# Performance work log

Hardware: AMD Instinct MI355X
Metric: run time of the kernel (lower is better)

Reference implementation:

```python
import jax, jax.numpy as jnp
import numpy as np

ALPHA = 0.5
PATH_LEN = 7  # 1 start entity + 3 (module, entity) hops
NUM_ENTITIES = 200000
EMBED = 128
NUM_MOD = 64
HIDDEN = 512
OUT_DIM = 64
BATCH = 8192


def setup_inputs() -> dict:
    key = jax.random.key(0)
    ks = jax.random.split(key, 8)
    stdv = 1.0 / np.sqrt(EMBED)
    return {
        "entity_embeds": jax.random.normal(ks[0], (NUM_ENTITIES, EMBED), jnp.float32) * 0.05,
        "W_mods": jax.random.uniform(ks[1], (NUM_MOD, EMBED, EMBED), jnp.float32, -stdv, stdv),
        "W1": jax.random.normal(ks[2], (HIDDEN, EMBED), jnp.float32) * stdv,
        "b1": jax.random.normal(ks[3], (HIDDEN,), jnp.float32) * 0.01,
        "W2": jax.random.normal(ks[4], (OUT_DIM, HIDDEN), jnp.float32) * (1.0 / np.sqrt(HIDDEN)),
        "b2": jax.random.normal(ks[5], (OUT_DIM,), jnp.float32) * 0.01,
        "entity_ids": jax.random.randint(ks[6], (BATCH, 4), 0, NUM_ENTITIES, jnp.int64 if jax.config.jax_enable_x64 else jnp.int32),
        "module_ids": jax.random.randint(ks[7], (BATCH, 3), 0, NUM_MOD, jnp.int64 if jax.config.jax_enable_x64 else jnp.int32),
    }


def reference(entity_embeds, W_mods, W1, b1, W2, b2, entity_ids, module_ids):
    # Batched version of ModuleNet.forward over a batch of fixed-length-7 paths.
    x = entity_embeds[entity_ids[:, 0]]  # [B, E] start entity embedding
    bias = x
    for h in range(3):  # hops over (module_id, entity_id) pairs
        Wm = W_mods[module_ids[:, h]]          # [B, E, E] per-row weight gather
        bias = entity_embeds[entity_ids[:, h + 1]]  # [B, E]
        x = jax.nn.relu(jnp.einsum('boi,bi->bo', Wm, x) + bias)
    w = 1.0 / (PATH_LEN * ALPHA)
    out = (1.0 - w) * bias + w * x  # [B, E]
    # classifier: Linear -> ReLU -> Linear
    h1 = jax.nn.relu(out @ W1.T + b1)
    logits = h1 @ W2.T + b2  # [B, OUT_DIM]
    return logits
```

## Files before the change

### kernel.cpp

```cpp
#include <hip/hip_runtime.h>

namespace {

typedef short bf16x8 __attribute__((ext_vector_type(8)));
typedef float f32x4 __attribute__((ext_vector_type(4)));

constexpr int BATCH = 8192;
constexpr int NMOD  = 64;
constexpr int CAP   = 256;
constexpr int CSTR  = 16;
constexpr float WB  = 1.0f / (7.0f * 0.5f);

constexpr size_t OFF_WHI = 0;
constexpr size_t OFF_WLO = 524288;
constexpr size_t OFF_XH0 = 1048576;
constexpr size_t OFF_XL0 = 1572864;
constexpr size_t OFF_XH1 = 2097152;
constexpr size_t OFF_XL1 = 2621440;
constexpr size_t OFF_W1H = 3145728;
constexpr size_t OFF_W1L = 3178496;
constexpr size_t OFF_W2H = 3211264;
constexpr size_t OFF_W2L = 3227648;
constexpr size_t OFF_CNT = 3244032;
constexpr size_t OFF_BKT = 3247104;

__device__ __forceinline__ ushort f2bf(float x) {
  unsigned u = __builtin_bit_cast(unsigned, x);
  u += 0x7FFFu + ((u >> 16) & 1u);
  return (ushort)(u >> 16);
}
__device__ __forceinline__ float bf2f(ushort h) {
  return __builtin_bit_cast(float, ((unsigned)h) << 16);
}
__device__ __forceinline__ void cvt8(const float* v, bf16x8& hi, bf16x8& lo) {
#pragma unroll
  for (int j = 0; j < 8; ++j) {
    const float x = v[j];
    const ushort h = f2bf(x);
    hi[j] = (short)h;
    lo[j] = (short)f2bf(x - bf2f(h));
  }
}

__global__ __launch_bounds__(256) void k_prep(const float* __restrict__ Wm,
                                              const float* __restrict__ W1,
                                              const float* __restrict__ W2,
                                              const int* __restrict__ mids,
                                              float* __restrict__ ws) {
  const int bx = blockIdx.x;
  const int tid = threadIdx.x;
  if (bx < 560) {
    const float* src;
    ushort *dh, *dl;
    size_t i8;
    if (bx < 512) {
      src = Wm; dh = (ushort*)(ws + OFF_WHI); dl = (ushort*)(ws + OFF_WLO);
      i8 = (size_t)bx * 256 + tid;
    } else if (bx < 544) {
      src = W1; dh = (ushort*)(ws + OFF_W1H); dl = (ushort*)(ws + OFF_W1L);
      i8 = (size_t)(bx - 512) * 256 + tid;
    } else {
      src = W2; dh = (ushort*)(ws + OFF_W2H); dl = (ushort*)(ws + OFF_W2L);
      i8 = (size_t)(bx - 544) * 256 + tid;
    }
    float v[8];
    *(float4*)&v[0] = *(const float4*)&src[i8 * 8];
    *(float4*)&v[4] = *(const float4*)&src[i8 * 8 + 4];
    bf16x8 hi, lo;
    cvt8(v, hi, lo);
    *(bf16x8*)&dh[i8 * 8] = hi;
    *(bf16x8*)&dl[i8 * 8] = lo;
  } else {
    const int idx = (bx - 560) * 256 + tid;
    if (idx < BATCH * 3) {
      const int b = idx / 3, h = idx - b * 3;
      const int m = mids[idx];
      int* cnt = (int*)(ws + OFF_CNT);
      int* bkt = (int*)(ws + OFF_BKT);
      const int pos = atomicAdd(&cnt[(h * NMOD + m) * CSTR], 1);
      bkt[(h * NMOD + m) * CAP + pos] = b;
    }
  }
}

template <int HOP>
__global__ __launch_bounds__(256, 2) void k_hop(const float* __restrict__ E,
                                                const int* __restrict__ eids,
                                                float* __restrict__ ws) {
  const int m = blockIdx.x >> 2, sl = blockIdx.x & 3;
  const int cn = ((const int*)(ws + OFF_CNT))[(HOP * NMOD + m) * CSTR];
  const int r0 = sl * 64;
  if (r0 >= cn) return;
  const int nr = min(64, cn - r0);

  __shared__ ushort wh[128 * 72];
  __shared__ ushort wl[128 * 72];
  __shared__ int rows[64], esrc[64], ebia[64];

  const int tid = threadIdx.x;
  const ushort* WhiG = (const ushort*)(ws + OFF_WHI) + (size_t)m * 16384;
  const ushort* WloG = (const ushort*)(ws + OFF_WLO) + (size_t)m * 16384;
  const int* bkt = (const int*)(ws + OFF_BKT) + (HOP * NMOD + m) * CAP + r0;
  const ushort* XHp = (const ushort*)(ws + (HOP == 2 ? OFF_XH1 : OFF_XH0));
  const ushort* XLp = (const ushort*)(ws + (HOP == 2 ? OFF_XL1 : OFF_XL0));
  ushort* XHn = (ushort*)(ws + (HOP == 1 ? OFF_XH1 : OFF_XH0));
  ushort* XLn = (ushort*)(ws + (HOP == 1 ? OFF_XL1 : OFF_XL0));

  if (tid < 64) {
    const int b = bkt[tid < nr ? tid : 0];
    rows[tid] = b;
    esrc[tid] = (HOP == 0) ? eids[b * 4] : b;
    ebia[tid] = eids[b * 4 + HOP + 1];
  }

  const int w = tid >> 6, l = tid & 63;
  const int lg = l >> 4, lr = l & 15;
  const int g0 = (w & 1) * 2, f0 = (w >> 1) * 4;

  f32x4 acc[2][4] = {};

#pragma unroll
  for (int p = 0; p < 2; ++p) {
    __syncthreads();
    for (int e = tid; e < 128 * 8; e += 256) {
      const int c = e >> 3, s = e & 7;
      *(bf16x8*)&wh[c * 72 + s * 8] =
          *(const bf16x8*)&WhiG[(size_t)c * 128 + p * 64 + s * 8];
      *(bf16x8*)&wl[c * 72 + s * 8] =
          *(const bf16x8*)&WloG[(size_t)c * 128 + p * 64 + s * 8];
    }
    __syncthreads();

    bf16x8 ah[2][2], al[2][2];
#pragma unroll
    for (int g = 0; g < 2; ++g) {
      const int row = (g0 + g) * 16 + lr;
#pragma unroll
      for (int s = 0; s < 2; ++s) {
        const int k0 = p * 64 + s * 32 + lg * 8;
        if (HOP == 0) {
          const float* sp = E + (size_t)esrc[row] * 128;
          float v[8];
          *(float4*)&v[0] = *(const float4*)&sp[k0];
          *(float4*)&v[4] = *(const float4*)&sp[k0 + 4];
          cvt8(v, ah[g][s], al[g][s]);
        } else {
          const size_t xo = (size_t)esrc[row] * 128 + k0;
          ah[g][s] = *(const bf16x8*)&XHp[xo];
          al[g][s] = *(const bf16x8*)&XLp[xo];
        }
      }
    }

#pragma unroll
    for (int f = 0; f < 4; ++f) {
      const int c = (f0 + f) * 16 + lr;
#pragma unroll
      for (int s = 0; s < 2; ++s) {
        const bf16x8 bh = *(const bf16x8*)&wh[c * 72 + s * 32 + lg * 8];
        const bf16x8 bl = *(const bf16x8*)&wl[c * 72 + s * 32 + lg * 8];
#pragma unroll
        for (int g = 0; g < 2; ++g) {
          acc[g][f] = __builtin_amdgcn_mfma_f32_16x16x32_bf16(ah[g][s], bh, acc[g][f], 0, 0, 0);
          acc[g][f] = __builtin_amdgcn_mfma_f32_16x16x32_bf16(al[g][s], bh, acc[g][f], 0, 0, 0);
          acc[g][f] = __builtin_amdgcn_mfma_f32_16x16x32_bf16(ah[g][s], bl, acc[g][f], 0, 0, 0);
        }
      }
    }
  }

#pragma unroll
  for (int g = 0; g < 2; ++g) {
#pragma unroll
    for (int q = 0; q < 4; ++q) {
      const int row = (g0 + g) * 16 + lg * 4 + q;
      if (row < nr) {
        const int b = rows[row];
        const float* bp = E + (size_t)ebia[row] * 128;
        const size_t ob = (size_t)b * 128;
#pragma unroll
        for (int f = 0; f < 4; ++f) {
          const int col = (f0 + f) * 16 + lr;
          const float bias = bp[col];
          float v = fmaxf(acc[g][f][q] + bias, 0.f);
          if (HOP == 2) v = (1.f - WB) * bias + WB * v;
          const ushort h = f2bf(v);
          XHn[ob + col] = h;
          XLn[ob + col] = f2bf(v - bf2f(h));
        }
      }
    }
  }
}

constexpr int HSTR = 520;
constexpr int WSTR = 136;
__global__ __launch_bounds__(256, 2) void k_mlp(const float* __restrict__ b1,
                                                const float* __restrict__ b2,
                                                float* __restrict__ ws,
                                                float* __restrict__ out) {
  __shared__ ushort w1h[64 * WSTR];
  __shared__ ushort w1l[64 * WSTR];
  __shared__ ushort hh[16 * HSTR];
  __shared__ ushort hl[16 * HSTR];
  const int tid = threadIdx.x;
  const int row0 = blockIdx.x * 16;
  const ushort* XH = (const ushort*)(ws + OFF_XH0);
  const ushort* XL = (const ushort*)(ws + OFF_XL0);
  const ushort* W1H = (const ushort*)(ws + OFF_W1H);
  const ushort* W1L = (const ushort*)(ws + OFF_W1L);
  const ushort* W2H = (const ushort*)(ws + OFF_W2H);
  const ushort* W2L = (const ushort*)(ws + OFF_W2L);

  const int w = tid >> 6, l = tid & 63;
  const int lg = l >> 4, lr = l & 15;

  bf16x8 ah[4], al[4];
#pragma unroll
  for (int s = 0; s < 4; ++s) {
    const size_t xo = (size_t)(row0 + lr) * 128 + s * 32 + lg * 8;
    ah[s] = *(const bf16x8*)&XH[xo];
    al[s] = *(const bf16x8*)&XL[xo];
  }

  for (int ch = 0; ch < 8; ++ch) {
    __syncthreads();
    for (int e = tid; e < 64 * 16; e += 256) {
      const int c = e >> 4, s8 = e & 15;
      const size_t go = (size_t)(ch * 64 + c) * 128 + s8 * 8;
      *(bf16x8*)&w1h[c * WSTR + s8 * 8] = *(const bf16x8*)&W1H[go];
      *(bf16x8*)&w1l[c * WSTR + s8 * 8] = *(const bf16x8*)&W1L[go];
    }
    __syncthreads();

    const int cl = w * 16 + lr;
    f32x4 a = {};
#pragma unroll
    for (int s = 0; s < 4; ++s) {
      const bf16x8 bh = *(const bf16x8*)&w1h[cl * WSTR + s * 32 + lg * 8];
      const bf16x8 bl = *(const bf16x8*)&w1l[cl * WSTR + s * 32 + lg * 8];
      a = __builtin_amdgcn_mfma_f32_16x16x32_bf16(ah[s], bh, a, 0, 0, 0);
      a = __builtin_amdgcn_mfma_f32_16x16x32_bf16(al[s], bh, a, 0, 0, 0);
      a = __builtin_amdgcn_mfma_f32_16x16x32_bf16(ah[s], bl, a, 0, 0, 0);
    }
    const int c = ch * 64 + w * 16 + lr;
    const float bb = b1[c];
#pragma unroll
    for (int q = 0; q < 4; ++q) {
      const int r = lg * 4 + q;
      const float v = fmaxf(a[q] + bb, 0.f);
      const ushort h = f2bf(v);
      hh[r * HSTR + c] = h;
      hl[r * HSTR + c] = f2bf(v - bf2f(h));
    }
  }
  __syncthreads();

  f32x4 acc2 = {};
#pragma unroll 4
  for (int s = 0; s < 16; ++s) {
    const size_t wo = (size_t)(w * 16 + lr) * 512 + s * 32 + lg * 8;
    const bf16x8 a2h = *(const bf16x8*)&W2H[wo];
    const bf16x8 a2l = *(const bf16x8*)&W2L[wo];
    const int ko = s * 32 + lg * 8;
    const bf16x8 b2h = *(const bf16x8*)&hh[lr * HSTR + ko];
    const bf16x8 b2l = *(const bf16x8*)&hl[lr * HSTR + ko];
    acc2 = __builtin_amdgcn_mfma_f32_16x16x32_bf16(a2h, b2h, acc2, 0, 0, 0);
    acc2 = __builtin_amdgcn_mfma_f32_16x16x32_bf16(a2l, b2h, acc2, 0, 0, 0);
    acc2 = __builtin_amdgcn_mfma_f32_16x16x32_bf16(a2h, b2l, acc2, 0, 0, 0);
  }
  const float4 bb2 = *(const float4*)&b2[w * 16 + lg * 4];
  float4 o;
  o.x = acc2[0] + bb2.x;
  o.y = acc2[1] + bb2.y;
  o.z = acc2[2] + bb2.z;
  o.w = acc2[3] + bb2.w;
  *(float4*)&out[(size_t)(row0 + lr) * 64 + w * 16 + lg * 4] = o;
}

}

extern "C" void kernel_launch(void* const* d_in, const int* in_sizes, int n_in,
                              void* d_out, int out_size, void* d_ws,
                              size_t ws_size, hipStream_t stream) {
  const float* E  = (const float*)d_in[0];
  const float* Wm = (const float*)d_in[1];
  const float* W1 = (const float*)d_in[2];
  const float* b1 = (const float*)d_in[3];
  const float* W2 = (const float*)d_in[4];
  const float* b2 = (const float*)d_in[5];
  const int* eids = (const int*)d_in[6];
  const int* mids = (const int*)d_in[7];
  float* out = (float*)d_out;
  float* ws = (float*)d_ws;

  (void)hipMemsetAsync((char*)d_ws + OFF_CNT * sizeof(float), 0,
                       192 * CSTR * sizeof(int), stream);
  k_prep<<<dim3(656), dim3(256), 0, stream>>>(Wm, W1, W2, mids, ws);
  k_hop<0><<<dim3(256), dim3(256), 0, stream>>>(E, eids, ws);
  k_hop<1><<<dim3(256), dim3(256), 0, stream>>>(E, eids, ws);
  k_hop<2><<<dim3(256), dim3(256), 0, stream>>>(E, eids, ws);
  k_mlp<<<dim3(512), dim3(256), 0, stream>>>(b1, b2, ws, out);
}
```

Baseline: 79.80 us.

## Fuse hop 0 and bucketing into prep kernel, replacing atomics with ballot compaction

Hop 0 now runs inside the prep kernel. Its blocks rebuild their own bucket rows by scanning module ids with ballot prefix sums and convert the module weights to hi/lo bf16 on the fly, so they no longer depend on the prepared workspace. Bucketing for hops 1 and 2 uses per-(hop, module) blocks with deterministic ballot compaction instead of atomics, which removes the memset. Together this drops one launch and one memset, but each block scans all 8192 ids, which adds redundant reads and serial loop work per block.

```diff
diff --git a/kernel.cpp b/kernel.cpp
--- a/kernel.cpp
+++ b/kernel.cpp
@@ -42,13 +42,18 @@
   }
 }
 
-__global__ __launch_bounds__(256) void k_prep(const float* __restrict__ Wm,
-                                              const float* __restrict__ W1,
-                                              const float* __restrict__ W2,
-                                              const int* __restrict__ mids,
-                                              float* __restrict__ ws) {
+__global__ __launch_bounds__(256, 2) void k_prep(
+    const float* __restrict__ E, const float* __restrict__ Wm,
+    const float* __restrict__ W1, const float* __restrict__ W2,
+    const int* __restrict__ eids, const int* __restrict__ mids,
+    float* __restrict__ ws) {
+  __shared__ ushort wh[128 * 72];
+  __shared__ ushort wl[128 * 72];
+  __shared__ int rows[64], esrc[64], ebia[64];
+  __shared__ int wsum[4];
   const int bx = blockIdx.x;
   const int tid = threadIdx.x;
+
   if (bx < 560) {
     const float* src;
     ushort *dh, *dl;
@@ -70,15 +75,145 @@
     cvt8(v, hi, lo);
     *(bf16x8*)&dh[i8 * 8] = hi;
     *(bf16x8*)&dl[i8 * 8] = lo;
-  } else {
-    const int idx = (bx - 560) * 256 + tid;
-    if (idx < BATCH * 3) {
-      const int b = idx / 3, h = idx - b * 3;
-      const int m = mids[idx];
-      int* cnt = (int*)(ws + OFF_CNT);
-      int* bkt = (int*)(ws + OFF_BKT);
-      const int pos = atomicAdd(&cnt[(h * NMOD + m) * CSTR], 1);
-      bkt[(h * NMOD + m) * CAP + pos] = b;
+    return;
+  }
+
+  if (bx < 688) {
+    const int hm64 = bx - 560;
+    const int h = 1 + (hm64 >> 6), m = hm64 & 63;
+    const int hm = h * NMOD + m;
+    int* cnt = (int*)(ws + OFF_CNT);
+    int* bkt = (int*)(ws + OFF_BKT) + hm * CAP;
+    const int wv = tid >> 6, ln = tid & 63;
+    int count = 0;
+    for (int it = 0; it < BATCH / 256; ++it) {
+      const int b = it * 256 + tid;
+      const bool hit = (mids[b * 3 + h] == m);
+      const unsigned long long mask = __ballot(hit);
+      const int pre = __popcll(mask & ((1ull << ln) - 1ull));
+      if (ln == 0) wsum[wv] = __popcll(mask);
+      __syncthreads();
+      int wbase = count;
+#pragma unroll
+      for (int u = 0; u < 4; ++u)
+        if (u < wv) wbase += wsum[u];
+      if (hit) bkt[wbase + pre] = b;
+      count += wsum[0] + wsum[1] + wsum[2] + wsum[3];
+      __syncthreads();
+    }
+    if (tid == 0) cnt[hm * CSTR] = count;
+    return;
+  }
+
+  const int t = bx - 688;
+  const int m = t >> 2, sl = t & 3;
+  const int r0 = sl * 64;
+  const int wv = tid >> 6, ln = tid & 63;
+
+  int count = 0;
+  for (int it = 0; it < BATCH / 256; ++it) {
+    const int b = it * 256 + tid;
+    const bool hit = (mids[b * 3] == m);
+    const unsigned long long mask = __ballot(hit);
+    const int pre = __popcll(mask & ((1ull << ln) - 1ull));
+    if (ln == 0) wsum[wv] = __popcll(mask);
+    __syncthreads();
+    int wbase = count;
+#pragma unroll
+    for (int u = 0; u < 4; ++u)
+      if (u < wv) wbase += wsum[u];
+    if (hit) {
+      const int rank = wbase + pre;
+      if (rank >= r0 && rank < r0 + 64) rows[rank - r0] = b;
+    }
+    count += wsum[0] + wsum[1] + wsum[2] + wsum[3];
+    __syncthreads();
+  }
+  const int cn = count;
+  if (r0 >= cn) return;
+  const int nr = min(64, cn - r0);
+
+  if (tid < 64) {
+    const int b = rows[tid < nr ? tid : 0];
+    rows[tid] = b;
+    esrc[tid] = eids[b * 4];
+    ebia[tid] = eids[b * 4 + 1];
+  }
+
+  const float* WmG = Wm + (size_t)m * 16384;
+  ushort* XHn = (ushort*)(ws + OFF_XH0);
+  ushort* XLn = (ushort*)(ws + OFF_XL0);
+  const int lg = ln >> 4, lr = ln & 15;
+  const int g0 = (wv & 1) * 2, f0 = (wv >> 1) * 4;
+
+  f32x4 acc[2][4] = {};
+#pragma unroll
+  for (int p = 0; p < 2; ++p) {
+    __syncthreads();
+    for (int e = tid; e < 128 * 8; e += 256) {
+      const int c = e >> 3, s = e & 7;
+      float v[8];
+      const float* sp = &WmG[(size_t)c * 128 + p * 64 + s * 8];
+      *(float4*)&v[0] = *(const float4*)&sp[0];
+      *(float4*)&v[4] = *(const float4*)&sp[4];
+      bf16x8 hi, lo;
+      cvt8(v, hi, lo);
+      *(bf16x8*)&wh[c * 72 + s * 8] = hi;
+      *(bf16x8*)&wl[c * 72 + s * 8] = lo;
+    }
+    __syncthreads();
+
+    bf16x8 ah[2][2], al[2][2];
+#pragma unroll
+    for (int g = 0; g < 2; ++g) {
+      const int row = (g0 + g) * 16 + lr;
+#pragma unroll
+      for (int s = 0; s < 2; ++s) {
+        const int k0 = p * 64 + s * 32 + lg * 8;
+        const float* sp = E + (size_t)esrc[row] * 128;
+        float v[8];
+        *(float4*)&v[0] = *(const float4*)&sp[k0];
+        *(float4*)&v[4] = *(const float4*)&sp[k0 + 4];
+        cvt8(v, ah[g][s], al[g][s]);
+      }
+    }
+
+#pragma unroll
+    for (int f = 0; f < 4; ++f) {
+      const int c = (f0 + f) * 16 + lr;
+#pragma unroll
+      for (int s = 0; s < 2; ++s) {
+        const bf16x8 bh = *(const bf16x8*)&wh[c * 72 + s * 32 + lg * 8];
+        const bf16x8 bl = *(const bf16x8*)&wl[c * 72 + s * 32 + lg * 8];
+#pragma unroll
+        for (int g = 0; g < 2; ++g) {
+          acc[g][f] = __builtin_amdgcn_mfma_f32_16x16x32_bf16(ah[g][s], bh, acc[g][f], 0, 0, 0);
+          acc[g][f] = __builtin_amdgcn_mfma_f32_16x16x32_bf16(al[g][s], bh, acc[g][f], 0, 0, 0);
+          acc[g][f] = __builtin_amdgcn_mfma_f32_16x16x32_bf16(ah[g][s], bl, acc[g][f], 0, 0, 0);
+        }
+      }
+    }
+  }
+
+#pragma unroll
+  for (int g = 0; g < 2; ++g) {
+#pragma unroll
+    for (int q = 0; q < 4; ++q) {
+      const int row = (g0 + g) * 16 + lg * 4 + q;
+      if (row < nr) {
+        const int b = rows[row];
+        const float* bp = E + (size_t)ebia[row] * 128;
+        const size_t ob = (size_t)b * 128;
+#pragma unroll
+        for (int f = 0; f < 4; ++f) {
+          const int col = (f0 + f) * 16 + lr;
+          const float bias = bp[col];
+          const float v = fmaxf(acc[g][f][q] + bias, 0.f);
+          const ushort h = f2bf(v);
+          XHn[ob + col] = h;
+          XLn[ob + col] = f2bf(v - bf2f(h));
+        }
+      }
     }
   }
 }
@@ -109,7 +244,7 @@
   if (tid < 64) {
     const int b = bkt[tid < nr ? tid : 0];
     rows[tid] = b;
-    esrc[tid] = (HOP == 0) ? eids[b * 4] : b;
+    esrc[tid] = b;
     ebia[tid] = eids[b * 4 + HOP + 1];
   }
 
@@ -138,17 +273,9 @@
 #pragma unroll
       for (int s = 0; s < 2; ++s) {
         const int k0 = p * 64 + s * 32 + lg * 8;
-        if (HOP == 0) {
-          const float* sp = E + (size_t)esrc[row] * 128;
-          float v[8];
-          *(float4*)&v[0] = *(const float4*)&sp[k0];
-          *(float4*)&v[4] = *(const float4*)&sp[k0 + 4];
-          cvt8(v, ah[g][s], al[g][s]);
-        } else {
-          const size_t xo = (size_t)esrc[row] * 128 + k0;
-          ah[g][s] = *(const bf16x8*)&XHp[xo];
-          al[g][s] = *(const bf16x8*)&XLp[xo];
-        }
+        const size_t xo = (size_t)esrc[row] * 128 + k0;
+        ah[g][s] = *(const bf16x8*)&XHp[xo];
+        al[g][s] = *(const bf16x8*)&XLp[xo];
       }
     }
 
@@ -294,10 +421,7 @@
   float* out = (float*)d_out;
   float* ws = (float*)d_ws;
 
-  (void)hipMemsetAsync((char*)d_ws + OFF_CNT * sizeof(float), 0,
-                       192 * CSTR * sizeof(int), stream);
-  k_prep<<<dim3(656), dim3(256), 0, stream>>>(Wm, W1, W2, mids, ws);
-  k_hop<0><<<dim3(256), dim3(256), 0, stream>>>(E, eids, ws);
+  k_prep<<<dim3(944), dim3(256), 0, stream>>>(E, Wm, W1, W2, eids, mids, ws);
   k_hop<1><<<dim3(256), dim3(256), 0, stream>>>(E, eids, ws);
   k_hop<2><<<dim3(256), dim3(256), 0, stream>>>(E, eids, ws);
   k_mlp<<<dim3(512), dim3(256), 0, stream>>>(b1, b2, ws, out);
```

New measurement: 82.33 us. 1.03x slower.
